# Performance work log

Hardware: AMD Instinct MI355X
Metric: run time of the kernel (lower is better)

Reference implementation:

```python
import jax, jax.numpy as jnp
from jax import lax
import numpy as np

B, T, F = 4, 16000, 512          # batch, frames, enc_num_feats
NB = 24                          # 3 stacks x 8 layers
DILS = [2 ** l for _ in range(3) for l in range(8)]


def _prelu(x, a):
    return jnp.where(x >= 0, x, a * x)


def _conv(x, w, stride=1, pad=0, dil=1, groups=1):
    # x: [B,C,T], w: [O, C//groups, K]
    return lax.conv_general_dilated(x, w, (stride,), [(pad, pad)], rhs_dilation=(dil,),
                                    dimension_numbers=('NCH', 'OIH', 'NCH'),
                                    feature_group_count=groups)


def _tconv(x, w, stride=1):
    # torch ConvTranspose1d, weight layout [in, out, k], padding=0
    k = w.shape[-1]
    wf = jnp.flip(w, -1).transpose(1, 0, 2)  # [out, in, k]
    return lax.conv_general_dilated(x, wf, (1,), [(k - 1, k - 1)], lhs_dilation=(stride,),
                                    dimension_numbers=('NCH', 'OIH', 'NCH'))


def _pw(x, w, b):
    # 1x1 conv as GEMM; w: [O,C], b: [O]
    return jnp.einsum('oc,bct->bot', w, x) + b[:, None]


def _branch(x, p):
    # encoder
    f = _conv(x, p['enc_w0'], stride=8)                       # [B,512,1999]
    f = _prelu(_conv(f, p['enc_w1']), p['enc_a'][0])          # [B,512,1997]
    f = _prelu(_conv(f, p['enc_w2']), p['enc_a'][1])          # [B,512,1995]
    # mask generator (TCN)
    o = _pw(f, p['mg_in_w'], p['mg_in_b'])                    # [B,128,t]
    for i in range(NB):
        d = DILS[i]
        h = _prelu(_pw(o, p['blk_w1'][i], p['blk_b1'][i]), p['blk_a1'][i])     # [B,32,t]
        h = _conv(h, p['blk_dw'][i][:, None, :], pad=d, dil=d, groups=32) + p['blk_db'][i][:, None]
        h = _prelu(h, p['blk_a2'][i])
        if i < NB - 1:  # last block has no residual path
            o = o + _pw(h, p['blk_rw'][i], p['blk_rb'][i])
        o = o + _pw(h, p['blk_sw'][i], p['blk_sb'][i])
    m = jax.nn.sigmoid(_pw(_prelu(o, p['mg_out_a']), p['mg_out_w'], p['mg_out_b']))  # [B,1024,t]
    b, _, t = f.shape
    m = m.reshape(b, 2, F, t)
    y = (m * f[:, None]).reshape(b * 2, F, t)
    # decoder
    y = _prelu(_tconv(y, p['dec_w1']), p['dec_a'][0])
    y = _prelu(_tconv(y, p['dec_w2']), p['dec_a'][1])
    y = _tconv(y, p['dec_w3'], stride=8)                      # [2B,1,T]
    return y.reshape(b, 2, -1)


_NAMES = ['x_real', 'x_imag', 'enc_w0', 'enc_w1', 'enc_w2', 'enc_a', 'mg_in_w', 'mg_in_b',
          'blk_w1', 'blk_b1', 'blk_a1', 'blk_dw', 'blk_db', 'blk_a2', 'blk_rw', 'blk_rb',
          'blk_sw', 'blk_sb', 'mg_out_a', 'mg_out_w', 'mg_out_b', 'dec_w1', 'dec_w2', 'dec_a', 'dec_w3']


def _forward(*args):
    p = dict(zip(_NAMES, args))
    out_r = _branch(p['x_real'], p)
    out_i = _branch(p['x_imag'], p)
    return jnp.stack([out_r, out_i])  # [2, B, 2, T]; axis0 = (real, imag)


def setup_inputs() -> dict:
    key = jax.random.key(0)
    ks = jax.random.split(key, 16)
    n = lambda k, s, sc: jax.random.normal(k, s, dtype=jnp.float32) * sc
    f32 = jnp.float32
    return {
        'x_real': jax.random.normal(ks[0], (B, 1, T), dtype=f32),
        'x_imag': jax.random.normal(ks[1], (B, 1, T), dtype=f32),
        'enc_w0': n(ks[2], (512, 1, 16), 0.1),
        'enc_w1': n(ks[3], (512, 512, 3), 0.03),
        'enc_w2': n(ks[4], (512, 512, 3), 0.03),
        'enc_a': jnp.full((2,), 0.25, f32),
        'mg_in_w': n(ks[5], (128, 512), 0.05),
        'mg_in_b': jnp.zeros((128,), f32),
        'blk_w1': n(ks[6], (NB, 32, 128), 0.08),
        'blk_b1': jnp.zeros((NB, 32), f32),
        'blk_a1': jnp.full((NB,), 0.25, f32),
        'blk_dw': n(ks[7], (NB, 32, 3), 0.2),
        'blk_db': jnp.zeros((NB, 32), f32),
        'blk_a2': jnp.full((NB,), 0.25, f32),
        'blk_rw': n(ks[8], (NB, 128, 32), 0.08),  # index NB-1 unused (no_residual)
        'blk_rb': jnp.zeros((NB, 128), f32),
        'blk_sw': n(ks[9], (NB, 128, 32), 0.08),
        'blk_sb': jnp.zeros((NB, 128), f32),
        'mg_out_a': jnp.asarray(0.25, f32),
        'mg_out_w': n(ks[10], (1024, 128), 0.08),
        'mg_out_b': jnp.zeros((1024,), f32),
        'dec_w1': n(ks[11], (512, 512, 3), 0.03),
        'dec_w2': n(ks[12], (512, 512, 3), 0.03),
        'dec_a': jnp.full((2,), 0.25, f32),
        'dec_w3': n(ks[13], (512, 1, 16), 0.1),
    }


def reference(x_real, x_imag, enc_w0, enc_w1, enc_w2, enc_a, mg_in_w, mg_in_b,
              blk_w1, blk_b1, blk_a1, blk_dw, blk_db, blk_a2, blk_rw, blk_rb,
              blk_sw, blk_sb, mg_out_a, mg_out_w, mg_out_b, dec_w1, dec_w2, dec_a, dec_w3):
    return _forward(x_real, x_imag, enc_w0, enc_w1, enc_w2, enc_a, mg_in_w, mg_in_b,
                    blk_w1, blk_b1, blk_a1, blk_dw, blk_db, blk_a2, blk_rw, blk_rb,
                    blk_sw, blk_sb, mg_out_a, mg_out_w, mg_out_b, dec_w1, dec_w2, dec_a, dec_w3)
```

## Files before the change

### kernel.cpp

```cpp
#include <hip/hip_runtime.h>
#include <hip/hip_cooperative_groups.h>

namespace cg = cooperative_groups;


typedef unsigned short u16;
typedef __attribute__((ext_vector_type(8))) short bf16x8_t;
typedef __attribute__((ext_vector_type(4))) float f32x4_t;

#define ST    2064
#define HALO  8
#define TR    2064
#define RHALO 8

#define U_F0H   0ULL
#define U_F1H   8454144ULL
#define F_F2    8454144ULL
#define F_D2    0ULL
#define U_YH    33816576ULL
#define U_D1H   50724864ULL
#define F_O     33816576ULL
#define F_G0    35930112ULL
#define F_G1    36458496ULL
#define F_W     36986880ULL
#define W_MGIN  0ULL
#define W_MGOUT 65536ULL
#define W_W1T   196608ULL
#define W_WSUMT 294912ULL
#define W_BSUM  393216ULL
#define U_WB    74766336ULL
#define F_FLAG  38956032ULL
#define F_G2    38964224ULL
#define F_G3    39492608ULL
#define U_W1B   74375168ULL
#define U_WSB   74563584ULL

#define WS_HI 0
#define WS_LO 5120
#define W1_HI 10240
#define W1_LO 14592
#define OB_HI 0
#define OB_LO 8704
#define HB_HI 0
#define HB_LO 2560

__device__ __forceinline__ float prelu_f(float x, float a) { return x >= 0.f ? x : a * x; }
__device__ __forceinline__ u16 f2b(float f) {
    unsigned u = __float_as_uint(f);
    return (u16)((u + 0x7FFF + ((u >> 16) & 1)) >> 16);
}
__device__ __forceinline__ float b2f(u16 h) {
    return __uint_as_float((unsigned)h << 16);
}
__device__ __forceinline__ void gload16(const void* g, void* l) {
    __builtin_amdgcn_global_load_lds(
        (const __attribute__((address_space(1))) unsigned*)g,
        (__attribute__((address_space(3))) unsigned*)l, 16, 0, 0);
}

__global__ __launch_bounds__(256) void prep_all(
    const float* __restrict__ ew1, const float* __restrict__ ew2,
    const float* __restrict__ dw1, const float* __restrict__ dw2,
    const float* __restrict__ mgin_w, const float* __restrict__ mgout_w,
    const float* __restrict__ bw1, const float* __restrict__ brw,
    const float* __restrict__ brb, const float* __restrict__ bsw,
    const float* __restrict__ bsb, float* __restrict__ wsf, u16* __restrict__ wsb,
    unsigned* __restrict__ flags)
{
    const int task = blockIdx.y;
    const int idx  = blockIdx.x * 256 + threadIdx.x;
    const int stride = gridDim.x * 256;
    if (task < 4) {
        const float* src = (task == 0) ? ew1 : (task == 1) ? ew2 : (task == 2) ? dw1 : dw2;
        u16* dst = wsb + U_WB + (size_t)task * 786432ULL;
        const bool dec = (task >= 2);
        for (int n = idx; n < 786432; n += stride) {
            int j = n >> 18, o = (n >> 9) & 511, c = n & 511;
            float v = dec ? src[(size_t)c * 1536 + o * 3 + (2 - j)]
                          : src[(size_t)o * 1536 + c * 3 + j];
            dst[n] = f2b(v);
        }
    } else if (task == 4) {
        float* dst = wsf + F_W + W_MGIN;
        for (int n = idx; n < 65536; n += stride) {
            int o = n & 127, c = n >> 7;
            dst[n] = mgin_w[(size_t)o * 512 + c];
        }
    } else if (task == 5) {
        float* dst = wsf + F_W + W_MGOUT;
        for (int n = idx; n < 131072; n += stride) {
            int m = n & 1023, c = n >> 10;
            dst[n] = mgout_w[(size_t)m * 128 + c];
        }
    } else if (task == 6) {
        float* dstf = wsf + F_W + W_W1T;
        for (int n = idx; n < 4096; n += stride) {
            int cc = n & 31, C = n >> 5;
            dstf[n] = bw1[(size_t)cc * 128 + C];
        }
        u16* dstb = wsb + U_W1B;
        for (int n = idx; n < 188416; n += stride) {
            int C = n & 127, cgi = (n >> 7) & 31, p = (n >> 12) & 1, ii = n >> 13;
            float v = bw1[(size_t)(ii + 1) * 4096 + cgi * 128 + C];
            u16 hh = f2b(v);
            if (p) hh = f2b(v - b2f(hh));
            dstb[n] = hh;
        }
    } else if (task == 7) {
        u16* dst = wsb + U_WSB;
        for (int n = idx; n < 196608; n += stride) {
            int cc = n & 31, C = (n >> 5) & 127, p = (n >> 12) & 1, i = n >> 13;
            float v = bsw[(size_t)i * 4096 + C * 32 + cc];
            if (i < 23) v += brw[(size_t)i * 4096 + C * 32 + cc];
            u16 hh = f2b(v);
            if (p) hh = f2b(v - b2f(hh));
            dst[n] = hh;
        }
    } else if (task == 8) {
        float* dst = wsf + F_W + W_BSUM;
        for (int n = idx; n < 3072; n += stride) {
            int i = n >> 7;
            float v = bsb[n];
            if (i < 23) v += brb[n];
            dst[n] = v;
        }
    } else if (task == 9) {
        const unsigned long long uoff[4] = { U_F0H, U_F1H, U_YH, U_D1H };
        const int nbArr[4]   = { 8, 8, 16, 16 };
        const int trArr[4]   = { 1999, 1997, 1995, 1997 };
#pragma unroll
        for (int z = 0; z < 4; z++) {
            unsigned* base = (unsigned*)(wsb + uoff[z]);
            const int nb = nbArr[z], Treal = trArr[z];
            const int prcnt = TR - Treal;
            const int total = nb * prcnt * 256;
            for (int n = idx; n < total; n += stride) {
                const int col = n & 255;
                const int r   = n >> 8;
                const int bb  = r / prcnt;
                const int pr  = r % prcnt;
                const int row = (pr < RHALO) ? pr : (Treal + pr);
                base[((size_t)bb * TR + row) * 256 + col] = 0u;
            }
        }
    } else {
        for (int n = idx; n < 4096; n += stride) flags[n] = 0u;
    }
}

__global__ __launch_bounds__(256) void enc0_kernel(
    const float* __restrict__ xr, const float* __restrict__ xi,
    const float* __restrict__ w0, u16* __restrict__ f0h)
{
    const int t  = blockIdx.x * 256 + threadIdx.x;
    const int c0 = blockIdx.y * 8;
    const int b  = blockIdx.z;
    if (t >= 1999) return;
    const float* x = (b < 4) ? (xr + (size_t)b * 16000) : (xi + (size_t)(b - 4) * 16000);
    float xv[16];
    const int base = t * 8;
#pragma unroll
    for (int k = 0; k < 16; k++) xv[k] = x[base + k];
    union { u16 u[8]; uint4 v; } p;
#pragma unroll
    for (int cq = 0; cq < 8; cq++) {
        const float* w = w0 + (size_t)(c0 + cq) * 16;
        float acc = 0.f;
#pragma unroll
        for (int k = 0; k < 16; k++) acc = fmaf(xv[k], w[k], acc);
        p.u[cq] = f2b(acc);
    }
    *(uint4*)&f0h[((size_t)b * TR + RHALO + t) * 512 + c0] = p.v;
}

template <int JOFF, int OUTF32>
__global__ __launch_bounds__(256) void conv_mfma(
    const u16* __restrict__ in, u16* __restrict__ out16, float* __restrict__ out32,
    const u16* __restrict__ wM, const float* __restrict__ alpha_p, int Tout)
{
    __shared__ __align__(16) u16 smem[17408];
    u16* As = smem;
    u16* Bs = smem + 12288;
    const int tid  = threadIdx.x;
    const int t0   = blockIdx.x * 128;
    const int ob   = blockIdx.y * 128;
    const int b    = blockIdx.z;
    const int l15  = tid & 15;
    const int quad = (tid >> 4) & 3;
    const int wave = tid >> 6;
    const int wm   = (wave & 1) * 64;
    const int wn   = (wave >> 1) * 64;
    const u16* inb = in + (size_t)b * TR * 512;
    const int wvb  = wave * 1024;

    f32x4_t acc[4][4];
#pragma unroll
    for (int i = 0; i < 4; i++)
#pragma unroll
        for (int k = 0; k < 4; k++) acc[i][k] = (f32x4_t){0.f, 0.f, 0.f, 0.f};

    for (int c0 = 0; c0 < 512; c0 += 32) {
#pragma unroll
        for (int k = 0; k < 6; k++) {
            const int v = k * 256 + tid;
            const int j = v >> 9, r = (v >> 2) & 127, c = v & 3;
            const int cg = c ^ ((r >> 1) & 3);
            gload16(&wM[((size_t)(j * 512 + ob + r)) * 512 + c0 + cg * 8],
                    (char*)As + k * 4096 + wvb);
        }
#pragma unroll
        for (int k = 0; k < 2; k++) {
            const int v = k * 256 + tid;
            const int r = v >> 2, c = v & 3;
            const int cg = c ^ ((r >> 1) & 3);
            gload16(&inb[(size_t)(RHALO + t0 + JOFF + r) * 512 + c0 + cg * 8],
                    (char*)Bs + k * 4096 + wvb);
        }
        if (tid < 16) {
            const int v = 512 + tid;
            const int r = v >> 2, c = v & 3;
            const int cg = c ^ ((r >> 1) & 3);
            gload16(&inb[(size_t)(RHALO + t0 + JOFF + r) * 512 + c0 + cg * 8],
                    (char*)Bs + 8192);
        }
        __syncthreads();
#pragma unroll
        for (int j = 0; j < 3; j++) {
            bf16x8_t aw[4], bi[4];
#pragma unroll
            for (int mf = 0; mf < 4; mf++) {
                const int row = wm + mf * 16 + l15;
                const int ch  = quad ^ ((row >> 1) & 3);
                aw[mf] = *(const bf16x8_t*)&As[j * 4096 + row * 32 + ch * 8];
            }
#pragma unroll
            for (int nf = 0; nf < 4; nf++) {
                const int row = wn + nf * 16 + l15 + j;
                const int ch  = quad ^ ((row >> 1) & 3);
                bi[nf] = *(const bf16x8_t*)&Bs[row * 32 + ch * 8];
            }
#pragma unroll
            for (int mf = 0; mf < 4; mf++)
#pragma unroll
                for (int nf = 0; nf < 4; nf++) {
                    if (OUTF32)
                        acc[mf][nf] = __builtin_amdgcn_mfma_f32_16x16x32_bf16(
                            bi[nf], aw[mf], acc[mf][nf], 0, 0, 0);
                    else
                        acc[mf][nf] = __builtin_amdgcn_mfma_f32_16x16x32_bf16(
                            aw[mf], bi[nf], acc[mf][nf], 0, 0, 0);
                }
        }
        __syncthreads();
    }

    const float alpha = *alpha_p;
    if (!OUTF32) {
        u16* tile = smem;
#pragma unroll
        for (int mf = 0; mf < 4; mf++)
#pragma unroll
            for (int nf = 0; nf < 4; nf++) {
                const int t_loc = wn + nf * 16 + l15;
                const int c_loc = wm + mf * 16 + quad * 4;
                f32x4_t a = acc[mf][nf];
                ushort4 s;
                s.x = f2b(prelu_f(a.x, alpha));
                s.y = f2b(prelu_f(a.y, alpha));
                s.z = f2b(prelu_f(a.z, alpha));
                s.w = f2b(prelu_f(a.w, alpha));
                *(ushort4*)&tile[t_loc * 136 + c_loc] = s;
            }
        __syncthreads();
        for (int v = tid; v < 2048; v += 256) {
            const int row = v >> 4, seg = v & 15;
            const int t = t0 + row;
            if (t < Tout)
                *(uint4*)&out16[((size_t)b * TR + RHALO + t) * 512 + ob + seg * 8] =
                    *(const uint4*)&tile[row * 136 + seg * 8];
        }
    } else {
#pragma unroll
        for (int mf = 0; mf < 4; mf++)
#pragma unroll
            for (int nf = 0; nf < 4; nf++) {
                const int o  = ob + wm + mf * 16 + l15;
                const int tb = t0 + wn + nf * 16 + quad * 4;
                f32x4_t a = acc[mf][nf];
                float v0 = prelu_f(a.x, alpha), v1 = prelu_f(a.y, alpha);
                float v2 = prelu_f(a.z, alpha), v3 = prelu_f(a.w, alpha);
                float* p = out32 + ((size_t)(b * 512 + o)) * ST + HALO + tb;
                if (tb + 3 < Tout) {
                    *(float4*)p = make_float4(v0, v1, v2, v3);
                } else {
                    if (tb + 0 < Tout) p[0] = v0;
                    if (tb + 1 < Tout) p[1] = v1;
                    if (tb + 2 < Tout) p[2] = v2;
                    if (tb + 3 < Tout) p[3] = v3;
                }
            }
    }
}

__global__ __launch_bounds__(256) void mgin_kernel(
    const float* __restrict__ f2, float* __restrict__ o_buf, float* __restrict__ g_out,
    const float* __restrict__ wT, const float* __restrict__ bias,
    const float* __restrict__ w1T0, const float* __restrict__ b1_0,
    const float* __restrict__ a1_0)
{
    __shared__ float Bs[16][64];
    __shared__ float As[16][128];
    __shared__ float o_lds[128][64];
    const int tid = threadIdx.x;
    const int t0  = blockIdx.x * 64;
    const int b   = blockIdx.y;
    const float* f2b_ = f2 + (size_t)b * 512 * ST + HALO + t0;

    float acc[8][4];
#pragma unroll
    for (int i = 0; i < 8; i++)
#pragma unroll
        for (int k = 0; k < 4; k++) acc[i][k] = 0.f;
    const int tx = tid & 15, ty = tid >> 4;

    for (int c0 = 0; c0 < 512; c0 += 16) {
        {
            int c = tid >> 4, p = tid & 15;
            *(float4*)(&Bs[c][p * 4]) = *(const float4*)(f2b_ + (size_t)(c0 + c) * ST + p * 4);
        }
#pragma unroll
        for (int r = 0; r < 2; r++) {
            int n4 = tid + r * 256;
            int c = n4 >> 5, m4 = n4 & 31;
            *(float4*)(&As[c][m4 * 4]) = *(const float4*)(wT + (size_t)(c0 + c) * 128 + m4 * 4);
        }
        __syncthreads();
#pragma unroll 2
        for (int c = 0; c < 16; c++) {
            float4 bv = *(const float4*)(&Bs[c][tx * 4]);
            float a[8];
            *(float4*)(&a[0]) = *(const float4*)(&As[c][ty * 8]);
            *(float4*)(&a[4]) = *(const float4*)(&As[c][ty * 8 + 4]);
#pragma unroll
            for (int oi = 0; oi < 8; oi++) {
                acc[oi][0] = fmaf(a[oi], bv.x, acc[oi][0]);
                acc[oi][1] = fmaf(a[oi], bv.y, acc[oi][1]);
                acc[oi][2] = fmaf(a[oi], bv.z, acc[oi][2]);
                acc[oi][3] = fmaf(a[oi], bv.w, acc[oi][3]);
            }
        }
        __syncthreads();
    }

    const int tb = t0 + tx * 4;
#pragma unroll
    for (int oi = 0; oi < 8; oi++) {
        const int o = ty * 8 + oi;
        const float bo = bias[o];
        float vv[4];
#pragma unroll
        for (int kk = 0; kk < 4; kk++) vv[kk] = acc[oi][kk] + bo;
        *(float4*)(&o_lds[o][tx * 4]) = make_float4(vv[0], vv[1], vv[2], vv[3]);
        float* orow = o_buf + (size_t)(b * 128 + o) * ST + HALO + tb;
        if (tb + 3 < 1995) {
            *(float4*)orow = make_float4(vv[0], vv[1], vv[2], vv[3]);
        } else {
#pragma unroll
            for (int kk = 0; kk < 4; kk++)
                if (tb + kk < 1995) orow[kk] = vv[kk];
        }
    }
    __syncthreads();

    const int t = tid & 63, cg_ = tid >> 6;
    const float a1 = *a1_0;
    float acc2[8];
#pragma unroll
    for (int q = 0; q < 8; q++) acc2[q] = b1_0[cg_ * 8 + q];
    for (int C = 0; C < 128; C++) {
        const float ov = o_lds[C][t];
        const float4* wr = (const float4*)(w1T0 + (size_t)C * 32 + cg_ * 8);
        float4 w0 = wr[0], w1 = wr[1];
        acc2[0] = fmaf(w0.x, ov, acc2[0]); acc2[1] = fmaf(w0.y, ov, acc2[1]);
        acc2[2] = fmaf(w0.z, ov, acc2[2]); acc2[3] = fmaf(w0.w, ov, acc2[3]);
        acc2[4] = fmaf(w1.x, ov, acc2[4]); acc2[5] = fmaf(w1.y, ov, acc2[5]);
        acc2[6] = fmaf(w1.z, ov, acc2[6]); acc2[7] = fmaf(w1.w, ov, acc2[7]);
    }
    const int tt = t0 + t;
    if (tt < 1995) {
#pragma unroll
        for (int q = 0; q < 8; q++)
            g_out[(size_t)(b * 32 + cg_ * 8 + q) * ST + HALO + tt] = prelu_f(acc2[q], a1);
    }
}

__device__ __forceinline__ void poll_acquire(const unsigned* flags, int b, int j,
                                             int k, unsigned target)
{
    int lo = j - k; if (lo < 0) lo = 0;
    int hi = j + k; if (hi > 31) hi = 31;
    for (int n = lo; n <= hi; n++) {
        if (n == j) continue;
        const unsigned* p = flags + ((b << 5) + n) * 16;
        while (__hip_atomic_load(p, __ATOMIC_RELAXED, __HIP_MEMORY_SCOPE_AGENT) < target)
            __builtin_amdgcn_s_sleep(2);
    }
    __builtin_amdgcn_fence(__ATOMIC_ACQUIRE, "agent");
}

__device__ __forceinline__ void store_pair_agent(float* dst, int trel, float v0, float v1)
{
    if (trel + 1 < 1995) {
        unsigned long long raw =
            ((unsigned long long)__float_as_uint(v1) << 32) | __float_as_uint(v0);
        __hip_atomic_store((unsigned long long*)dst, raw,
                           __ATOMIC_RELAXED, __HIP_MEMORY_SCOPE_AGENT);
    } else if (trel < 1995) {
        __hip_atomic_store(dst, v0, __ATOMIC_RELAXED, __HIP_MEMORY_SCOPE_AGENT);
    }
}

__global__ __launch_bounds__(512) void tcn_fused(
    float* __restrict__ g0, float* __restrict__ g1,
    float* __restrict__ g2, float* __restrict__ g3,
    float* __restrict__ o_buf,
    const float* __restrict__ dw_all, const float* __restrict__ db_all,
    const float* __restrict__ a2_all,
    const u16* __restrict__ wsb16, const float* __restrict__ bsum_all,
    const u16* __restrict__ w1b16, const float* __restrict__ b1_all,
    const float* __restrict__ a1_all, unsigned* __restrict__ wflag)
{
    __shared__ __align__(16) u16  wbuf[18944];
    __shared__ __align__(16) u16  hbuf[5120];
    __shared__ __align__(16) u16  ob16[17408];
    __shared__ __align__(16) float g_lds[2][2176];
    __shared__ __align__(16) float halo_lds[8320];

    const int tid = threadIdx.x;
    const int blk = blockIdx.x;
    const int b   = blk & 7;
    const int jt  = blk >> 3;
    const int t0  = jt * 64;
    float* gbuf[4] = { g0, g1, g2, g3 };

    const int wv   = tid >> 6;
    const int l15  = tid & 15;
    const int quad = (tid >> 4) & 3;
    const int Cb   = wv * 16 + quad * 4;

    f32x4_t o_acc[4];
#pragma unroll
    for (int k = 0; k < 4; k++)
#pragma unroll
        for (int r = 0; r < 4; r++)
            o_acc[k][r] = o_buf[((size_t)(b * 128 + Cb + r)) * ST + HALO + t0 + k * 16 + l15];
    {
        int cc = tid >> 4, seg = tid & 15;
        *(float4*)&g_lds[0][cc * 68 + seg * 4] =
            *(const float4*)&g0[((size_t)(b * 32 + cc)) * ST + HALO + t0 + seg * 4];
    }

    for (int i = 0; i < 24; i++) {
        const int dil  = 1 << (i & 7);
        const int dil2 = (dil < 2) ? 2 : dil;
        const int k_rd = (dil > 64) ? 2 : 1;
        const float* gin_g = gbuf[i & 3];
        float* gout_g      = gbuf[(i + 1) & 3];
        float* gin_lds  = g_lds[i & 1];
        float* gout_lds = g_lds[(i + 1) & 1];

        {
            const u16* wsg = wsb16 + (size_t)i * 8192;
#pragma unroll
            for (int k = 0; k < 2; k++) {
                int c = tid + k * 512;
                int p = c >> 9, r = (c >> 2) & 127, s = c & 3;
                *(uint4*)&wbuf[(p ? WS_LO : WS_HI) + r * 40 + s * 8] =
                    *(const uint4*)&wsg[c * 8];
            }
            if (i < 23) {
                const u16* w1g = w1b16 + (size_t)i * 8192;
#pragma unroll
                for (int k = 0; k < 2; k++) {
                    int c = tid + k * 512;
                    int p = c >> 9, cgi = (c >> 4) & 31, s = c & 15;
                    *(uint4*)&wbuf[(p ? W1_LO : W1_HI) + cgi * 136 + s * 8] =
                        *(const uint4*)&w1g[c * 8];
                }
            }
        }

        if (i > 0 && tid == 0) poll_acquire(wflag, b, jt, k_rd, (unsigned)i);
        __syncthreads();

        {
            const int dsh = (dil2 >= 128) ? 7 : (dil2 >= 64) ? 6 : (dil2 >= 32) ? 5
                          : (dil2 >= 16) ? 4 : (dil2 >= 8) ? 3 : (dil2 >= 4) ? 2 : 1;
            const int total = 32 << dsh;
            for (int n = tid; n < total; n += 512) {
                const int cc = n >> dsh;
                const int pi = n & (dil2 - 1);
                const int hc = pi * 2;
                const int tg = (hc < dil2) ? (t0 - dil2 + hc) : (t0 + 64 + hc - dil2);
                float v0 = 0.f, v1 = 0.f;
                const float* src = gin_g + ((size_t)(b * 32 + cc)) * ST + HALO + tg;
                if (tg >= 0 && tg + 1 < 1995) {
                    unsigned long long raw = __hip_atomic_load(
                        (const unsigned long long*)src,
                        __ATOMIC_RELAXED, __HIP_MEMORY_SCOPE_AGENT);
                    v0 = __uint_as_float((unsigned)raw);
                    v1 = __uint_as_float((unsigned)(raw >> 32));
                } else {
                    if (tg >= 0 && tg < 1995)
                        v0 = __hip_atomic_load(src, __ATOMIC_RELAXED,
                                               __HIP_MEMORY_SCOPE_AGENT);
                    if (tg + 1 >= 0 && tg + 1 < 1995)
                        v1 = __hip_atomic_load(src + 1, __ATOMIC_RELAXED,
                                               __HIP_MEMORY_SCOPE_AGENT);
                }
                halo_lds[cc * 260 + hc]     = v0;
                halo_lds[cc * 260 + hc + 1] = v1;
            }
        }
        __syncthreads();

        {
            const float a2 = a2_all[i];
            const int t = tid & 63, cc0 = (tid >> 6) * 4;
            const int tt = t0 + t;
            ushort4 hi4, lo4;
            u16 hs[4], ls[4];
#pragma unroll
            for (int q = 0; q < 4; q++) {
                const int cc = cc0 + q;
                const float w0 = dw_all[i * 96 + cc * 3 + 0];
                const float w1v = dw_all[i * 96 + cc * 3 + 1];
                const float w2 = dw_all[i * 96 + cc * 3 + 2];
                const float ctr = gin_lds[cc * 68 + t];
                float lo = 0.f, hi = 0.f;
                const int tm = tt - dil;
                if (tm >= 0)
                    lo = (tm >= t0) ? gin_lds[cc * 68 + (tm - t0)]
                                    : halo_lds[cc * 260 + (tm - t0 + dil2)];
                const int tp = tt + dil;
                if (tp < 1995)
                    hi = (tp < t0 + 64) ? gin_lds[cc * 68 + (tp - t0)]
                                        : halo_lds[cc * 260 + (dil2 + tp - t0 - 64)];
                float s = db_all[i * 32 + cc] + w1v * ctr;
                s = fmaf(w0, lo, s);
                s = fmaf(w2, hi, s);
                const float hval = prelu_f(s, a2);
                const u16 hh = f2b(hval);
                hs[q] = hh;
                ls[q] = f2b(hval - b2f(hh));
            }
            hi4.x = hs[0]; hi4.y = hs[1]; hi4.z = hs[2]; hi4.w = hs[3];
            lo4.x = ls[0]; lo4.y = ls[1]; lo4.z = ls[2]; lo4.w = ls[3];
            *(ushort4*)&hbuf[HB_HI + t * 40 + cc0] = hi4;
            *(ushort4*)&hbuf[HB_LO + t * 40 + cc0] = lo4;
        }
        __syncthreads();

        {
            const bf16x8_t a_hi = *(const bf16x8_t*)&wbuf[WS_HI + (wv * 16 + l15) * 40 + quad * 8];
            const bf16x8_t a_lo = *(const bf16x8_t*)&wbuf[WS_LO + (wv * 16 + l15) * 40 + quad * 8];
            const float4 bs4 = *(const float4*)&bsum_all[i * 128 + Cb];
#pragma unroll
            for (int k = 0; k < 4; k++) {
                const bf16x8_t b_hi = *(const bf16x8_t*)&hbuf[HB_HI + (k * 16 + l15) * 40 + quad * 8];
                const bf16x8_t b_lo = *(const bf16x8_t*)&hbuf[HB_LO + (k * 16 + l15) * 40 + quad * 8];
                f32x4_t acc = o_acc[k];
                acc = __builtin_amdgcn_mfma_f32_16x16x32_bf16(a_lo, b_hi, acc, 0, 0, 0);
                acc = __builtin_amdgcn_mfma_f32_16x16x32_bf16(a_hi, b_lo, acc, 0, 0, 0);
                acc = __builtin_amdgcn_mfma_f32_16x16x32_bf16(a_hi, b_hi, acc, 0, 0, 0);
                acc.x += bs4.x; acc.y += bs4.y; acc.z += bs4.z; acc.w += bs4.w;
                o_acc[k] = acc;
            }
        }

        if (i == 23) break;

#pragma unroll
        for (int k = 0; k < 4; k++) {
            ushort4 hi4, lo4;
            u16 hs[4], ls[4];
#pragma unroll
            for (int r = 0; r < 4; r++) {
                const float v = o_acc[k][r];
                const u16 hh = f2b(v);
                hs[r] = hh;
                ls[r] = f2b(v - b2f(hh));
            }
            hi4.x = hs[0]; hi4.y = hs[1]; hi4.z = hs[2]; hi4.w = hs[3];
            lo4.x = ls[0]; lo4.y = ls[1]; lo4.z = ls[2]; lo4.w = ls[3];
            const int t_loc = k * 16 + l15;
            *(ushort4*)&ob16[OB_HI + t_loc * 136 + Cb] = hi4;
            *(ushort4*)&ob16[OB_LO + t_loc * 136 + Cb] = lo4;
        }
        __syncthreads();

        {
            const int cgb = (wv & 1) * 16;
            const int tb  = (wv >> 1) * 16;
            const float4 b14 = *(const float4*)&b1_all[(i + 1) * 32 + cgb + quad * 4];
            f32x4_t ga = (f32x4_t){b14.x, b14.y, b14.z, b14.w};
            f32x4_t gc = (f32x4_t){0.f, 0.f, 0.f, 0.f};
#pragma unroll
            for (int slab = 0; slab < 4; slab++) {
                const bf16x8_t wa_hi = *(const bf16x8_t*)&wbuf[W1_HI + (cgb + l15) * 136 + slab * 32 + quad * 8];
                const bf16x8_t wa_lo = *(const bf16x8_t*)&wbuf[W1_LO + (cgb + l15) * 136 + slab * 32 + quad * 8];
                const bf16x8_t obh   = *(const bf16x8_t*)&ob16[OB_HI + (tb + l15) * 136 + slab * 32 + quad * 8];
                const bf16x8_t obl   = *(const bf16x8_t*)&ob16[OB_LO + (tb + l15) * 136 + slab * 32 + quad * 8];
                if (slab & 1) {
                    gc = __builtin_amdgcn_mfma_f32_16x16x32_bf16(wa_lo, obh, gc, 0, 0, 0);
                    gc = __builtin_amdgcn_mfma_f32_16x16x32_bf16(wa_hi, obl, gc, 0, 0, 0);
                    gc = __builtin_amdgcn_mfma_f32_16x16x32_bf16(wa_hi, obh, gc, 0, 0, 0);
                } else {
                    ga = __builtin_amdgcn_mfma_f32_16x16x32_bf16(wa_lo, obh, ga, 0, 0, 0);
                    ga = __builtin_amdgcn_mfma_f32_16x16x32_bf16(wa_hi, obl, ga, 0, 0, 0);
                    ga = __builtin_amdgcn_mfma_f32_16x16x32_bf16(wa_hi, obh, ga, 0, 0, 0);
                }
            }
            const float a1 = a1_all[i + 1];
#pragma unroll
            for (int r = 0; r < 4; r++) {
                const int cgr = cgb + quad * 4 + r;
                gout_lds[cgr * 68 + tb + l15] = prelu_f(ga[r] + gc[r], a1);
            }
        }
        __syncthreads();

        {
            const int dnext = 1 << ((i + 1) & 7);
            int md2 = (dnext > 64) ? 64 : dnext;
            if (md2 < 2) md2 = 2;
            if (md2 >= 64) {
                for (int n = tid; n < 1024; n += 512) {
                    const int cc = n >> 5, pi = n & 31;
                    const int lt = pi * 2;
                    float* dst = gout_g + ((size_t)(b * 32 + cc)) * ST + HALO + t0 + lt;
                    store_pair_agent(dst, t0 + lt,
                                     gout_lds[cc * 68 + lt], gout_lds[cc * 68 + lt + 1]);
                }
            } else {
                const int msh = (md2 >= 32) ? 5 : (md2 >= 16) ? 4 : (md2 >= 8) ? 3
                              : (md2 >= 4) ? 2 : 1;
                const int total = 32 << msh;
                for (int n = tid; n < total; n += 512) {
                    const int cc = n >> msh;
                    const int pi = n & (md2 - 1);
                    const int hc = pi * 2;
                    const int lt = (hc < md2) ? hc : (64 - 2 * md2 + hc);
                    float* dst = gout_g + ((size_t)(b * 32 + cc)) * ST + HALO + t0 + lt;
                    store_pair_agent(dst, t0 + lt,
                                     gout_lds[cc * 68 + lt], gout_lds[cc * 68 + lt + 1]);
                }
            }
        }
        __syncthreads();

        if (tid == 0)
            __hip_atomic_store(&wflag[((b << 5) + jt) * 16], (unsigned)(i + 1),
                               __ATOMIC_RELAXED, __HIP_MEMORY_SCOPE_AGENT);
    }

#pragma unroll
    for (int k = 0; k < 4; k++)
#pragma unroll
        for (int r = 0; r < 4; r++)
            o_buf[((size_t)(b * 128 + Cb + r)) * ST + HALO + t0 + k * 16 + l15] = o_acc[k][r];
}

__global__ __launch_bounds__(256) void mask_kernel(
    const float* __restrict__ o_buf, const float* __restrict__ f2, u16* __restrict__ yh,
    const float* __restrict__ wT, const float* __restrict__ mb,
    const float* __restrict__ a_out_p)
{
    __shared__ __align__(16) char smem[65536];
    float (*o_lds)[64]  = (float (*)[64])smem;
    float (*w_lds)[256] = (float (*)[256])(smem + 32768);
    u16* tile = (u16*)smem;

    const int tid = threadIdx.x;
    const int t0  = blockIdx.x * 64;
    const int m0  = blockIdx.y * 256;
    const int b   = blockIdx.z;
    const float ao = *a_out_p;

#pragma unroll
    for (int r = 0; r < 8; r++) {
        int n4 = tid + r * 256;
        int C = n4 >> 4, p = n4 & 15;
        float4 v = *(const float4*)(o_buf + (size_t)(b * 128 + C) * ST + HALO + t0 + p * 4);
        v.x = prelu_f(v.x, ao); v.y = prelu_f(v.y, ao);
        v.z = prelu_f(v.z, ao); v.w = prelu_f(v.w, ao);
        *(float4*)(&o_lds[C][p * 4]) = v;
    }

    float acc[16][4];
#pragma unroll
    for (int i = 0; i < 16; i++)
#pragma unroll
        for (int k = 0; k < 4; k++) acc[i][k] = 0.f;
    const int tx = tid & 15, my = tid >> 4;

    for (int C0 = 0; C0 < 128; C0 += 32) {
#pragma unroll
        for (int r = 0; r < 8; r++) {
            int n4 = tid + r * 256;
            int c = n4 >> 6, m4 = n4 & 63;
            *(float4*)(&w_lds[c][m4 * 4]) =
                *(const float4*)(wT + (size_t)(C0 + c) * 1024 + m0 + m4 * 4);
        }
        __syncthreads();
#pragma unroll 2
        for (int c = 0; c < 32; c++) {
            float4 bv = *(const float4*)(&o_lds[C0 + c][tx * 4]);
            float a[16];
            *(float4*)(&a[0])  = *(const float4*)(&w_lds[c][my * 16 + 0]);
            *(float4*)(&a[4])  = *(const float4*)(&w_lds[c][my * 16 + 4]);
            *(float4*)(&a[8])  = *(const float4*)(&w_lds[c][my * 16 + 8]);
            *(float4*)(&a[12]) = *(const float4*)(&w_lds[c][my * 16 + 12]);
#pragma unroll
            for (int mm = 0; mm < 16; mm++) {
                acc[mm][0] = fmaf(a[mm], bv.x, acc[mm][0]);
                acc[mm][1] = fmaf(a[mm], bv.y, acc[mm][1]);
                acc[mm][2] = fmaf(a[mm], bv.z, acc[mm][2]);
                acc[mm][3] = fmaf(a[mm], bv.w, acc[mm][3]);
            }
        }
        __syncthreads();
    }

    const int tb = t0 + tx * 4;
#pragma unroll
    for (int mm = 0; mm < 16; mm++) {
        const int mi = m0 + my * 16 + mm;
        const float bb = mb[mi];
        const int F = mi & 511;
        const float* f2row = f2 + (size_t)(b * 512 + F) * ST + HALO + tb;
#pragma unroll
        for (int kk = 0; kk < 4; kk++) {
            const float mval = 1.f / (1.f + __expf(-(acc[mm][kk] + bb)));
            acc[mm][kk] = mval * f2row[kk];
        }
    }
#pragma unroll
    for (int kk = 0; kk < 4; kk++) {
        const int row = tx * 4 + kk;
#pragma unroll
        for (int half = 0; half < 2; half++) {
            union { u16 u[8]; uint4 v; } p;
#pragma unroll
            for (int q = 0; q < 8; q++) p.u[q] = f2b(acc[half * 8 + q][kk]);
            *(uint4*)&tile[row * 280 + my * 16 + half * 8] = p.v;
        }
    }
    __syncthreads();
    const int F0 = m0 & 511, sIdx = m0 >> 9;
    u16* ybase = yh + ((size_t)(b * 2 + sIdx) * TR) * 512;
    for (int i = tid; i < 2048; i += 256) {
        const int row = i >> 5, seg = i & 31;
        const int t = t0 + row;
        if (t < 1995)
            *(uint4*)&ybase[(size_t)(RHALO + t) * 512 + F0 + seg * 8] =
                *(const uint4*)&tile[row * 280 + seg * 8];
    }
}

__global__ __launch_bounds__(256) void dec3_kernel(
    const float* __restrict__ d2, const float* __restrict__ w3, float* __restrict__ out)
{
    __shared__ float tile[512][34];
    const int tid = threadIdx.x;
    const int bb  = blockIdx.y;
    const int tau0 = blockIdx.x * 256;
    const int tbase = (tau0 >> 3) - 1;
    const float* src = d2 + (size_t)bb * 512 * ST + HALO + tbase;
    for (int n = tid; n < 512 * 34; n += 256) {
        int o = n / 34, i = n % 34;
        const int tg = tbase + i;
        tile[o][i] = (tg >= 0 && tg < 1999) ? src[(size_t)o * ST + i] : 0.f;
    }
    __syncthreads();

    const int tau = tau0 + tid;
    if (tau >= 16000) return;
    const int k1 = tau & 7;
    const int t1l = (tid >> 3) + 1;
    float acc = 0.f;
#pragma unroll 8
    for (int o = 0; o < 512; o++) {
        acc = fmaf(tile[o][t1l],     w3[o * 16 + k1],     acc);
        acc = fmaf(tile[o][t1l - 1], w3[o * 16 + 8 + k1], acc);
    }
    const int p = bb >> 1, s = bb & 1;
    out[(size_t)(p * 2 + s) * 16000 + tau] = acc;
}

extern "C" void kernel_launch(void* const* d_in, const int* in_sizes, int n_in,
                              void* d_out, int out_size, void* d_ws, size_t ws_size,
                              hipStream_t stream)
{
    (void)in_sizes; (void)n_in; (void)out_size; (void)ws_size;
    float* ws  = (float*)d_ws;
    u16*   wsu = (u16*)d_ws;
    const float* x_real   = (const float*)d_in[0];
    const float* x_imag   = (const float*)d_in[1];
    const float* enc_w0   = (const float*)d_in[2];
    const float* enc_w1   = (const float*)d_in[3];
    const float* enc_w2   = (const float*)d_in[4];
    const float* enc_a    = (const float*)d_in[5];
    const float* mg_in_w  = (const float*)d_in[6];
    const float* mg_in_b  = (const float*)d_in[7];
    const float* blk_w1   = (const float*)d_in[8];
    const float* blk_b1   = (const float*)d_in[9];
    const float* blk_a1   = (const float*)d_in[10];
    const float* blk_dw   = (const float*)d_in[11];
    const float* blk_db   = (const float*)d_in[12];
    const float* blk_a2   = (const float*)d_in[13];
    const float* blk_rw   = (const float*)d_in[14];
    const float* blk_rb   = (const float*)d_in[15];
    const float* blk_sw   = (const float*)d_in[16];
    const float* blk_sb   = (const float*)d_in[17];
    const float* mg_out_a = (const float*)d_in[18];
    const float* mg_out_w = (const float*)d_in[19];
    const float* mg_out_b = (const float*)d_in[20];
    const float* dec_w1   = (const float*)d_in[21];
    const float* dec_w2   = (const float*)d_in[22];
    const float* dec_a    = (const float*)d_in[23];
    const float* dec_w3   = (const float*)d_in[24];
    float* out = (float*)d_out;

    u16*   f0h   = wsu + U_F0H;
    u16*   f1h   = wsu + U_F1H;
    float* f2    = ws  + F_F2;
    float* d2    = ws  + F_D2;
    u16*   yh    = wsu + U_YH;
    u16*   d1h   = wsu + U_D1H;
    float* obuf  = ws  + F_O;
    float* g0    = ws  + F_G0;
    float* g1    = ws  + F_G1;
    float* g2    = ws  + F_G2;
    float* g3    = ws  + F_G3;
    float* WF    = ws  + F_W;
    u16*   WB    = wsu + U_WB;
    unsigned* flags = (unsigned*)(ws + F_FLAG);

    const dim3 blk(256);

    prep_all<<<dim3(64, 11), blk, 0, stream>>>(enc_w1, enc_w2, dec_w1, dec_w2,
        mg_in_w, mg_out_w, blk_w1, blk_rw, blk_rb, blk_sw, blk_sb, ws, wsu, flags);

    enc0_kernel<<<dim3(8, 64, 8), blk, 0, stream>>>(x_real, x_imag, enc_w0, f0h);

    conv_mfma<0, 0><<<dim3(16, 4, 8), blk, 0, stream>>>(
        f0h, f1h, nullptr, WB + 0 * 786432, enc_a + 0, 1997);
    conv_mfma<0, 1><<<dim3(16, 4, 8), blk, 0, stream>>>(
        f1h, nullptr, f2, WB + 1 * 786432, enc_a + 1, 1995);

    mgin_kernel<<<dim3(32, 8), blk, 0, stream>>>(f2, obuf, g0, WF + W_MGIN, mg_in_b,
        WF + W_W1T, blk_b1, blk_a1);

    {
        const float* dwp   = blk_dw;
        const float* dbp   = blk_db;
        const float* a2p   = blk_a2;
        const u16*   wsbp  = wsu + U_WSB;
        const float* bsump = WF + W_BSUM;
        const u16*   w1bp  = wsu + U_W1B;
        const float* b1p   = blk_b1;
        const float* a1p   = blk_a1;
        unsigned* flg = flags;
        void* args[] = { &g0, &g1, &g2, &g3, &obuf,
                         (void*)&dwp, (void*)&dbp, (void*)&a2p,
                         (void*)&wsbp, (void*)&bsump, (void*)&w1bp,
                         (void*)&b1p, (void*)&a1p, &flg };
        (void)hipLaunchCooperativeKernel((void*)tcn_fused, dim3(256), dim3(512),
                                         args, 0, stream);
    }

    mask_kernel<<<dim3(32, 4, 8), blk, 0, stream>>>(obuf, f2, yh,
        WF + W_MGOUT, mg_out_b, mg_out_a);

    conv_mfma<-2, 0><<<dim3(16, 4, 16), blk, 0, stream>>>(
        yh, d1h, nullptr, WB + 2 * 786432, dec_a + 0, 1997);
    conv_mfma<-2, 1><<<dim3(16, 4, 16), blk, 0, stream>>>(
        d1h, nullptr, d2, WB + 3 * 786432, dec_a + 1, 1999);

    dec3_kernel<<<dim3(63, 16), blk, 0, stream>>>(d2, dec_w3, out);
}
```

Measured before the change: 758.8 us.

## Move mask-generator output GEMM to bf16x3 split MFMA

The mask kernel's 1024x128 pointwise GEMM is moved from scalar FP32 FMAs to MFMA bf16 instructions. Weights are pre-split on the device into hi/lo bf16 pairs, and activations are split the same way in LDS. Three MFMAs per tile (hi*hi, hi*lo, lo*hi) approximate FP32 accuracy. This trades some precision and extra prep work for matrix-core throughput, and the epilogue gathers f2 with a less coalesced access pattern.

```diff
diff --git a/kernel.cpp b/kernel.cpp
--- a/kernel.cpp
+++ b/kernel.cpp
@@ -32,6 +32,7 @@
 #define F_FLAG  38956032ULL
 #define F_G2    38964224ULL
 #define F_G3    39492608ULL
+#define U_MKB   74104832ULL
 #define U_W1B   74375168ULL
 #define U_WSB   74563584ULL
 
@@ -87,10 +88,13 @@
             dst[n] = mgin_w[(size_t)o * 512 + c];
         }
     } else if (task == 5) {
-        float* dst = wsf + F_W + W_MGOUT;
-        for (int n = idx; n < 131072; n += stride) {
-            int m = n & 1023, c = n >> 10;
-            dst[n] = mgout_w[(size_t)m * 128 + c];
+        u16* dst = wsb + U_MKB;
+        for (int n = idx; n < 262144; n += stride) {
+            int C = n & 127, m = (n >> 7) & 1023, p = n >> 17;
+            float v = mgout_w[(size_t)m * 128 + C];
+            u16 hh = f2b(v);
+            if (p) hh = f2b(v - b2f(hh));
+            dst[n] = hh;
         }
     } else if (task == 6) {
         float* dstf = wsf + F_W + W_W1T;
@@ -673,98 +677,111 @@
 
 __global__ __launch_bounds__(256) void mask_kernel(
     const float* __restrict__ o_buf, const float* __restrict__ f2, u16* __restrict__ yh,
-    const float* __restrict__ wT, const float* __restrict__ mb,
+    const u16* __restrict__ wA, const float* __restrict__ mb,
     const float* __restrict__ a_out_p)
 {
-    __shared__ __align__(16) char smem[65536];
-    float (*o_lds)[64]  = (float (*)[64])smem;
-    float (*w_lds)[256] = (float (*)[256])(smem + 32768);
-    u16* tile = (u16*)smem;
-
-    const int tid = threadIdx.x;
-    const int t0  = blockIdx.x * 64;
-    const int m0  = blockIdx.y * 256;
-    const int b   = blockIdx.z;
+    __shared__ __align__(16) u16 smem[33792];
+    u16* As = smem;
+    u16* ob = smem + 16384;
+
+    const int tid  = threadIdx.x;
+    const int t0   = blockIdx.x * 64;
+    const int m0   = blockIdx.y * 256;
+    const int b    = blockIdx.z;
     const float ao = *a_out_p;
-
-#pragma unroll
-    for (int r = 0; r < 8; r++) {
-        int n4 = tid + r * 256;
-        int C = n4 >> 4, p = n4 & 15;
-        float4 v = *(const float4*)(o_buf + (size_t)(b * 128 + C) * ST + HALO + t0 + p * 4);
-        v.x = prelu_f(v.x, ao); v.y = prelu_f(v.y, ao);
-        v.z = prelu_f(v.z, ao); v.w = prelu_f(v.w, ao);
-        *(float4*)(&o_lds[C][p * 4]) = v;
-    }
-
-    float acc[16][4];
-#pragma unroll
-    for (int i = 0; i < 16; i++)
-#pragma unroll
-        for (int k = 0; k < 4; k++) acc[i][k] = 0.f;
-    const int tx = tid & 15, my = tid >> 4;
-
-    for (int C0 = 0; C0 < 128; C0 += 32) {
-#pragma unroll
-        for (int r = 0; r < 8; r++) {
-            int n4 = tid + r * 256;
-            int c = n4 >> 6, m4 = n4 & 63;
-            *(float4*)(&w_lds[c][m4 * 4]) =
-                *(const float4*)(wT + (size_t)(C0 + c) * 1024 + m0 + m4 * 4);
-        }
-        __syncthreads();
-#pragma unroll 2
-        for (int c = 0; c < 32; c++) {
-            float4 bv = *(const float4*)(&o_lds[C0 + c][tx * 4]);
-            float a[16];
-            *(float4*)(&a[0])  = *(const float4*)(&w_lds[c][my * 16 + 0]);
-            *(float4*)(&a[4])  = *(const float4*)(&w_lds[c][my * 16 + 4]);
-            *(float4*)(&a[8])  = *(const float4*)(&w_lds[c][my * 16 + 8]);
-            *(float4*)(&a[12]) = *(const float4*)(&w_lds[c][my * 16 + 12]);
-#pragma unroll
-            for (int mm = 0; mm < 16; mm++) {
-                acc[mm][0] = fmaf(a[mm], bv.x, acc[mm][0]);
-                acc[mm][1] = fmaf(a[mm], bv.y, acc[mm][1]);
-                acc[mm][2] = fmaf(a[mm], bv.z, acc[mm][2]);
-                acc[mm][3] = fmaf(a[mm], bv.w, acc[mm][3]);
-            }
-        }
-        __syncthreads();
-    }
-
-    const int tb = t0 + tx * 4;
-#pragma unroll
-    for (int mm = 0; mm < 16; mm++) {
-        const int mi = m0 + my * 16 + mm;
-        const float bb = mb[mi];
-        const int F = mi & 511;
-        const float* f2row = f2 + (size_t)(b * 512 + F) * ST + HALO + tb;
-#pragma unroll
-        for (int kk = 0; kk < 4; kk++) {
-            const float mval = 1.f / (1.f + __expf(-(acc[mm][kk] + bb)));
-            acc[mm][kk] = mval * f2row[kk];
-        }
-    }
-#pragma unroll
-    for (int kk = 0; kk < 4; kk++) {
-        const int row = tx * 4 + kk;
-#pragma unroll
-        for (int half = 0; half < 2; half++) {
-            union { u16 u[8]; uint4 v; } p;
-#pragma unroll
-            for (int q = 0; q < 8; q++) p.u[q] = f2b(acc[half * 8 + q][kk]);
-            *(uint4*)&tile[row * 280 + my * 16 + half * 8] = p.v;
-        }
-    }
+    const int l15  = tid & 15;
+    const int quad = (tid >> 4) & 3;
+    const int wave = tid >> 6;
+    const int wm   = wave * 64;
+
+    {
+        const int C = tid >> 1, th = (tid & 1) * 32;
+        const float* orow = o_buf + (size_t)(b * 128 + C) * ST + HALO + t0 + th;
+#pragma unroll
+        for (int q = 0; q < 8; q++) {
+            float4 v = *(const float4*)(orow + q * 4);
+            const float vv[4] = {v.x, v.y, v.z, v.w};
+#pragma unroll
+            for (int j = 0; j < 4; j++) {
+                const float pv = prelu_f(vv[j], ao);
+                const u16 hh = f2b(pv);
+                const int t = th + q * 4 + j;
+                ob[OB_HI + t * 136 + C] = hh;
+                ob[OB_LO + t * 136 + C] = f2b(pv - b2f(hh));
+            }
+        }
+    }
+
+    f32x4_t acc[4][4];
+#pragma unroll
+    for (int mf = 0; mf < 4; mf++)
+#pragma unroll
+        for (int nf = 0; nf < 4; nf++) acc[mf][nf] = (f32x4_t){0.f, 0.f, 0.f, 0.f};
+
+    for (int ks = 0; ks < 4; ks++) {
+#pragma unroll
+        for (int k = 0; k < 8; k++) {
+            const int v = k * 256 + tid;
+            const int p = v >> 10, r = (v >> 2) & 255, c = v & 3;
+            const int cg = c ^ ((r >> 1) & 3);
+            gload16(&wA[(size_t)p * 131072 + (size_t)(m0 + r) * 128 + ks * 32 + cg * 8],
+                    (char*)As + k * 4096 + wave * 1024);
+        }
+        __syncthreads();
+        bf16x8_t ah[4], al[4], bh[4], bl[4];
+#pragma unroll
+        for (int mf = 0; mf < 4; mf++) {
+            const int row = wm + mf * 16 + l15;
+            const int ch  = quad ^ ((row >> 1) & 3);
+            ah[mf] = *(const bf16x8_t*)&As[row * 32 + ch * 8];
+            al[mf] = *(const bf16x8_t*)&As[8192 + row * 32 + ch * 8];
+        }
+#pragma unroll
+        for (int nf = 0; nf < 4; nf++) {
+            const int rt = nf * 16 + l15;
+            bh[nf] = *(const bf16x8_t*)&ob[OB_HI + rt * 136 + ks * 32 + quad * 8];
+            bl[nf] = *(const bf16x8_t*)&ob[OB_LO + rt * 136 + ks * 32 + quad * 8];
+        }
+#pragma unroll
+        for (int mf = 0; mf < 4; mf++)
+#pragma unroll
+            for (int nf = 0; nf < 4; nf++) {
+                acc[mf][nf] = __builtin_amdgcn_mfma_f32_16x16x32_bf16(al[mf], bh[nf], acc[mf][nf], 0, 0, 0);
+                acc[mf][nf] = __builtin_amdgcn_mfma_f32_16x16x32_bf16(ah[mf], bl[nf], acc[mf][nf], 0, 0, 0);
+                acc[mf][nf] = __builtin_amdgcn_mfma_f32_16x16x32_bf16(ah[mf], bh[nf], acc[mf][nf], 0, 0, 0);
+            }
+        __syncthreads();
+    }
+
+    const int F0 = m0 & 511, sIdx = m0 >> 9;
+    u16* tile = smem;
+#pragma unroll
+    for (int mf = 0; mf < 4; mf++)
+#pragma unroll
+        for (int nf = 0; nf < 4; nf++) {
+            const int tl = nf * 16 + l15;
+            u16 sv[4];
+#pragma unroll
+            for (int r = 0; r < 4; r++) {
+                const int mloc = wm + mf * 16 + quad * 4 + r;
+                const float x = acc[mf][nf][r] + mb[m0 + mloc];
+                const float mval = 1.f / (1.f + __expf(-x));
+                const float y = mval *
+                    f2[(size_t)(b * 512 + F0 + mloc) * ST + HALO + t0 + tl];
+                sv[r] = f2b(y);
+            }
+            ushort4 s;
+            s.x = sv[0]; s.y = sv[1]; s.z = sv[2]; s.w = sv[3];
+            *(ushort4*)&tile[tl * 264 + wm + mf * 16 + quad * 4] = s;
+        }
     __syncthreads();
-    const int F0 = m0 & 511, sIdx = m0 >> 9;
     u16* ybase = yh + ((size_t)(b * 2 + sIdx) * TR) * 512;
-    for (int i = tid; i < 2048; i += 256) {
-        const int row = i >> 5, seg = i & 31;
+    for (int v = tid; v < 2048; v += 256) {
+        const int row = v >> 5, seg = v & 31;
         const int t = t0 + row;
         if (t < 1995)
             *(uint4*)&ybase[(size_t)(RHALO + t) * 512 + F0 + seg * 8] =
-                *(const uint4*)&tile[row * 280 + seg * 8];
+                *(const uint4*)&tile[row * 264 + seg * 8];
     }
 }
 
@@ -881,7 +898,7 @@
     }
 
     mask_kernel<<<dim3(32, 4, 8), blk, 0, stream>>>(obuf, f2, yh,
-        WF + W_MGOUT, mg_out_b, mg_out_a);
+        wsu + U_MKB, mg_out_b, mg_out_a);
 
     conv_mfma<-2, 0><<<dim3(16, 4, 16), blk, 0, stream>>>(
         yh, d1h, nullptr, WB + 2 * 786432, dec_a + 0, 1997);
```

After: 715.0 us. -5.8%, faster.
